# Kernel optimization log

Measured on AMD Instinct MI355X. Metric: run time of the kernel, lower is better.

Reference implementation:

```python
import jax, jax.numpy as jnp
import numpy as np

G, NA, C, NMAX = 32, 1024, 4, 6   # graphs, atoms/graph, latent charge channels, k-grid extent
SIGMA = 1.0                        # Gaussian smearing width (Angstrom)
BOX_L = 20.0


def _kgrid_integers(nmax):
    """All integer triples in [-nmax, nmax]^3 excluding the origin. [K, 3]"""
    r = np.arange(-nmax, nmax + 1)
    n = np.stack(np.meshgrid(r, r, r, indexing='ij'), axis=-1).reshape(-1, 3)
    n = n[np.any(n != 0, axis=1)]
    return jnp.asarray(n, dtype=jnp.float32)  # [K=2196, 3]


def setup_inputs() -> dict:
    key = jax.random.key(0)
    k1, k2, k3 = jax.random.split(key, 3)
    pos = jax.random.uniform(k1, (G * NA, 3), dtype=jnp.float32) * BOX_L
    q = jax.random.normal(k2, (G * NA, C), dtype=jnp.float32) * 0.1
    # near-cubic cells with a small random strain (keeps them invertible)
    cell = jnp.eye(3, dtype=jnp.float32) * BOX_L + 0.1 * jax.random.normal(k3, (G, 3, 3), dtype=jnp.float32)
    batch = jnp.repeat(jnp.arange(G, dtype=jnp.int32), NA)  # sorted segment ids
    return {"q": q, "pos": pos, "cell": cell, "batch": batch}


def reference(q, pos, cell, batch):
    """Latent Ewald reciprocal-space sum.

    E_lr[g] = 1/(2 V_g) * sum_{k != 0} 4*pi/k^2 * exp(-sigma^2 k^2 / 2) * sum_c |S_c(k)|^2
    with S_c(k) = sum_{i in graph g} q_ic exp(i k . r_i).

    Segments are equal-sized and sorted (batch = repeat(arange(G), NA)), so the
    per-graph segment reduction is expressed as a reshape + batched einsum.
    """
    del batch  # layout is encoded by the reshape below (equal-sized sorted segments)
    nvec = _kgrid_integers(NMAX)                         # [K, 3]
    # reciprocal lattice rows: b_i with a_i . b_j = 2*pi*delta_ij
    recip = 2.0 * jnp.pi * jnp.swapaxes(jnp.linalg.inv(cell), -1, -2)  # [G, 3, 3]
    kvec = jnp.einsum('kj,gjd->gkd', nvec, recip)        # [G, K, 3]
    k2 = jnp.sum(kvec * kvec, axis=-1)                   # [G, K]
    vol = jnp.abs(jnp.linalg.det(cell))                  # [G]

    posg = pos.reshape(G, NA, 3)
    qg = q.reshape(G, NA, C)

    phase = jnp.einsum('gnd,gkd->gnk', posg, kvec)       # [G, NA, K]
    cosph = jnp.cos(phase)
    sinph = jnp.sin(phase)
    s_re = jnp.einsum('gnc,gnk->gkc', qg, cosph)         # [G, K, C]
    s_im = jnp.einsum('gnc,gnk->gkc', qg, sinph)
    s2 = jnp.sum(s_re * s_re + s_im * s_im, axis=-1)     # [G, K]

    w = 4.0 * jnp.pi * jnp.exp(-0.5 * (SIGMA ** 2) * k2) / jnp.maximum(k2, 1e-12)
    e_lr = jnp.sum(w * s2, axis=-1) / (2.0 * vol)        # [G]
    return e_lr
```

## Files before the change

kernel.cpp:

```cpp
#include <hip/hip_runtime.h>
#include <math.h>

#define G      32
#define NA     1024
#define C      4
#define KHALF  1098
#define KSLICES 18
#define WAVES  8
#define BLOCK  (WAVES * 64)
#define APW    (NA / WAVES)

typedef float f32x2 __attribute__((ext_vector_type(2)));
typedef float f32x4 __attribute__((ext_vector_type(4)));
typedef float f32x8 __attribute__((ext_vector_type(8)));

__global__ __launch_bounds__(256)
void prepack_kernel(const float* __restrict__ q,
                    const float* __restrict__ pos,
                    float* __restrict__ ws)
{
    const int a = blockIdx.x * 256 + threadIdx.x;
    if (a < G * NA) {
        f32x4 p4 = { pos[a * 3 + 0], pos[a * 3 + 1], pos[a * 3 + 2], 0.f };
        const f32x4 qa = *reinterpret_cast<const f32x4*>(q + (size_t)a * 4);
        f32x4* w = reinterpret_cast<f32x4*>(ws + (size_t)a * 8);
        w[0] = p4;
        w[1] = qa;
    }
}

#define LOAD4(R0, R1, R2, R3, P) do {                                      \
    asm volatile("s_load_dwordx8 %0, %1, 0x0"  : "=s"(R0) : "s"(P));        \
    asm volatile("s_load_dwordx8 %0, %1, 0x20" : "=s"(R1) : "s"(P));        \
    asm volatile("s_load_dwordx8 %0, %1, 0x40" : "=s"(R2) : "s"(P));        \
    asm volatile("s_load_dwordx8 %0, %1, 0x60" : "=s"(R3) : "s"(P));        \
} while (0)

#define WAIT4(R0, R1, R2, R3)                                              \
    asm volatile("s_waitcnt lgkmcnt(0)"                                     \
                 : "+s"(R0), "+s"(R1), "+s"(R2), "+s"(R3))

__global__ __launch_bounds__(BLOCK)
void ewald_recip_kernel(const float* __restrict__ ws,
                        const float* __restrict__ cell,
                        float* __restrict__ out)
{
    __shared__ float s_red[WAVES][64][8];

    const int b    = blockIdx.x;
    const int g    = b / KSLICES;
    const int ks   = b % KSLICES;
    const int t    = threadIdx.x;
    const int wave = t >> 6;
    const int lane = t & 63;

    const float* M = cell + (size_t)g * 9;
    const float m00 = M[0], m01 = M[1], m02 = M[2];
    const float m10 = M[3], m11 = M[4], m12 = M[5];
    const float m20 = M[6], m21 = M[7], m22 = M[8];
    const float c00 =  (m11 * m22 - m12 * m21);
    const float c01 = -(m10 * m22 - m12 * m20);
    const float c02 =  (m10 * m21 - m11 * m20);
    const float c10 = -(m01 * m22 - m02 * m21);
    const float c11 =  (m00 * m22 - m02 * m20);
    const float c12 = -(m00 * m21 - m01 * m20);
    const float c20 =  (m01 * m12 - m02 * m11);
    const float c21 = -(m00 * m12 - m02 * m10);
    const float c22 =  (m00 * m11 - m01 * m10);
    const float det    = m00 * c00 + m01 * c01 + m02 * c02;
    const float invdet = 1.0f / det;

    const int  kk    = ks * 64 + lane;
    const bool valid = (kk < KHALF);
    int n1, n2, n3;
    if (kk < 1014) {
        n1 = 1 + kk / 169;
        const int r = kk - (n1 - 1) * 169;
        n2 = r / 13 - 6;
        n3 = r - (r / 13) * 13 - 6;
    } else if (kk < 1092) {
        const int j = kk - 1014;
        n1 = 0;
        n2 = 1 + j / 13;
        n3 = j - (j / 13) * 13 - 6;
    } else {
        n1 = 0; n2 = 0;
        n3 = kk - 1091;
    }
    const float fn1 = (float)n1, fn2 = (float)n2, fn3 = (float)n3;

    const float kr0 = (fn1 * c00 + fn2 * c10 + fn3 * c20) * invdet;
    const float kr1 = (fn1 * c01 + fn2 * c11 + fn3 * c21) * invdet;
    const float kr2 = (fn1 * c02 + fn2 * c12 + fn3 * c22) * invdet;

    f32x2 aR01 = {0.f, 0.f}, aR23 = {0.f, 0.f};
    f32x2 aI01 = {0.f, 0.f}, aI23 = {0.f, 0.f};

    const unsigned wvByte = (unsigned)__builtin_amdgcn_readfirstlane(wave * APW * 32);
    const char* pa = reinterpret_cast<const char*>(ws)
                   + (size_t)g * NA * 32 + wvByte;

    auto comp = [&](const f32x8& rec) {
        const float ph = fmaf(rec[0], kr0, fmaf(rec[1], kr1, rec[2] * kr2));
        const float u  = __builtin_amdgcn_fractf(ph);
        const float sn = __builtin_amdgcn_sinf(u);
        const float cs = __builtin_amdgcn_cosf(u);
        const f32x2 cs2 = {cs, cs};
        const f32x2 sn2 = {sn, sn};
        const f32x2 q01 = {rec[4], rec[5]};
        const f32x2 q23 = {rec[6], rec[7]};
        aR01 = __builtin_elementwise_fma(q01, cs2, aR01);
        aR23 = __builtin_elementwise_fma(q23, cs2, aR23);
        aI01 = __builtin_elementwise_fma(q01, sn2, aI01);
        aI23 = __builtin_elementwise_fma(q23, sn2, aI23);
    };

    {
        f32x8 A0, A1, A2, A3, B0, B1, B2, B3;
        LOAD4(A0, A1, A2, A3, pa);  pa += 128;
        #pragma unroll 1
        for (int it = 0; it < 15; ++it) {
            WAIT4(A0, A1, A2, A3);
            LOAD4(B0, B1, B2, B3, pa);  pa += 128;
            comp(A0); comp(A1); comp(A2); comp(A3);
            WAIT4(B0, B1, B2, B3);
            LOAD4(A0, A1, A2, A3, pa);  pa += 128;
            comp(B0); comp(B1); comp(B2); comp(B3);
        }
        WAIT4(A0, A1, A2, A3);
        LOAD4(B0, B1, B2, B3, pa);
        comp(A0); comp(A1); comp(A2); comp(A3);
        WAIT4(B0, B1, B2, B3);
        comp(B0); comp(B1); comp(B2); comp(B3);
    }

    {
        float* rp = s_red[wave][lane];
        rp[0] = aR01.x; rp[1] = aR01.y; rp[2] = aR23.x; rp[3] = aR23.y;
        rp[4] = aI01.x; rp[5] = aI01.y; rp[6] = aI23.x; rp[7] = aI23.y;
    }
    __syncthreads();

    if (t < 64) {
        float r0 = 0.f, r1 = 0.f, r2 = 0.f, r3 = 0.f;
        float i0 = 0.f, i1 = 0.f, i2 = 0.f, i3 = 0.f;
        #pragma unroll
        for (int w = 0; w < WAVES; ++w) {
            const float* p = s_red[w][lane];
            r0 += p[0]; r1 += p[1]; r2 += p[2]; r3 += p[3];
            i0 += p[4]; i1 += p[5]; i2 += p[6]; i3 += p[7];
        }
        const float s2 = r0 * r0 + r1 * r1 + r2 * r2 + r3 * r3
                       + i0 * i0 + i1 * i1 + i2 * i2 + i3 * i3;
        const float kk2 = kr0 * kr0 + kr1 * kr1 + kr2 * kr2;
        const float fourpi2 = 4.0f * (float)M_PI * (float)M_PI;
        const float k2 = fourpi2 * kk2;
        const float wt = 4.0f * (float)M_PI * __expf(-0.5f * k2) / fmaxf(k2, 1e-12f);
        float contrib = valid ? wt * s2 : 0.0f;
        #pragma unroll
        for (int off = 32; off > 0; off >>= 1)
            contrib += __shfl_down(contrib, off, 64);
        if (lane == 0)
            atomicAdd(&out[g], contrib * fabsf(invdet));
    }
}

extern "C" void kernel_launch(void* const* d_in, const int* in_sizes, int n_in,
                              void* d_out, int out_size, void* d_ws, size_t ws_size,
                              hipStream_t stream) {
    const float* q    = (const float*)d_in[0];
    const float* pos  = (const float*)d_in[1];
    const float* cell = (const float*)d_in[2];
    float* out = (float*)d_out;
    float* ws  = (float*)d_ws;

    hipMemsetAsync(out, 0, G * sizeof(float), stream);

    prepack_kernel<<<(G * NA + 255) / 256, 256, 0, stream>>>(q, pos, ws);

    dim3 grid(G * KSLICES);
    dim3 block(BLOCK);
    ewald_recip_kernel<<<grid, block, 0, stream>>>(ws, cell, out);
}
```

Before: 83.95 us.

## Split atom dimension across blocks and add a separate reduction kernel

After: 85.16 us. Within noise of the previous version (+1.4%).

```diff
diff --git a/kernel.cpp b/kernel.cpp
--- a/kernel.cpp
+++ b/kernel.cpp
@@ -3,12 +3,15 @@
 
 #define G      32
 #define NA     1024
-#define C      4
 #define KHALF  1098
 #define KSLICES 18
+#define KSLOT  (KSLICES * 64)
 #define WAVES  8
 #define BLOCK  (WAVES * 64)
-#define APW    (NA / WAVES)
+#define ASPLIT 4
+#define APW    (NA / (WAVES * ASPLIT))
+
+#define REC_FLOATS (G * NA * 8)
 
 typedef float f32x2 __attribute__((ext_vector_type(2)));
 typedef float f32x4 __attribute__((ext_vector_type(4)));
@@ -40,39 +43,8 @@
     asm volatile("s_waitcnt lgkmcnt(0)"                                     \
                  : "+s"(R0), "+s"(R1), "+s"(R2), "+s"(R3))
 
-__global__ __launch_bounds__(BLOCK)
-void ewald_recip_kernel(const float* __restrict__ ws,
-                        const float* __restrict__ cell,
-                        float* __restrict__ out)
-{
-    __shared__ float s_red[WAVES][64][8];
-
-    const int b    = blockIdx.x;
-    const int g    = b / KSLICES;
-    const int ks   = b % KSLICES;
-    const int t    = threadIdx.x;
-    const int wave = t >> 6;
-    const int lane = t & 63;
-
-    const float* M = cell + (size_t)g * 9;
-    const float m00 = M[0], m01 = M[1], m02 = M[2];
-    const float m10 = M[3], m11 = M[4], m12 = M[5];
-    const float m20 = M[6], m21 = M[7], m22 = M[8];
-    const float c00 =  (m11 * m22 - m12 * m21);
-    const float c01 = -(m10 * m22 - m12 * m20);
-    const float c02 =  (m10 * m21 - m11 * m20);
-    const float c10 = -(m01 * m22 - m02 * m21);
-    const float c11 =  (m00 * m22 - m02 * m20);
-    const float c12 = -(m00 * m21 - m01 * m20);
-    const float c20 =  (m01 * m12 - m02 * m11);
-    const float c21 = -(m00 * m12 - m02 * m10);
-    const float c22 =  (m00 * m11 - m01 * m10);
-    const float det    = m00 * c00 + m01 * c01 + m02 * c02;
-    const float invdet = 1.0f / det;
-
-    const int  kk    = ks * 64 + lane;
-    const bool valid = (kk < KHALF);
-    int n1, n2, n3;
+__device__ __forceinline__ void decode_k(int kk, int& n1, int& n2, int& n3)
+{
     if (kk < 1014) {
         n1 = 1 + kk / 169;
         const int r = kk - (n1 - 1) * 169;
@@ -87,6 +59,46 @@
         n1 = 0; n2 = 0;
         n3 = kk - 1091;
     }
+}
+
+#define CELL_COFACTORS(M)                                                  \
+    const float m00 = M[0], m01 = M[1], m02 = M[2];                         \
+    const float m10 = M[3], m11 = M[4], m12 = M[5];                         \
+    const float m20 = M[6], m21 = M[7], m22 = M[8];                         \
+    const float c00 =  (m11 * m22 - m12 * m21);                             \
+    const float c01 = -(m10 * m22 - m12 * m20);                             \
+    const float c02 =  (m10 * m21 - m11 * m20);                             \
+    const float c10 = -(m01 * m22 - m02 * m21);                             \
+    const float c11 =  (m00 * m22 - m02 * m20);                             \
+    const float c12 = -(m00 * m21 - m01 * m20);                             \
+    const float c20 =  (m01 * m12 - m02 * m11);                             \
+    const float c21 = -(m00 * m12 - m02 * m10);                             \
+    const float c22 =  (m00 * m11 - m01 * m10);                             \
+    const float det    = m00 * c00 + m01 * c01 + m02 * c02;                 \
+    const float invdet = 1.0f / det;
+
+__global__ __launch_bounds__(BLOCK)
+void ewald_partial_kernel(const float* __restrict__ ws,
+                          const float* __restrict__ cell,
+                          float* __restrict__ part)
+{
+    __shared__ float s_red[WAVES][64][8];
+
+    const int b    = blockIdx.x;
+    const int g    = b / (KSLICES * ASPLIT);
+    const int rem  = b % (KSLICES * ASPLIT);
+    const int ks   = rem / ASPLIT;
+    const int as   = rem % ASPLIT;
+    const int t    = threadIdx.x;
+    const int wave = t >> 6;
+    const int lane = t & 63;
+
+    const float* M = cell + (size_t)g * 9;
+    CELL_COFACTORS(M);
+
+    const int kk = ks * 64 + lane;
+    int n1, n2, n3;
+    decode_k(kk, n1, n2, n3);
     const float fn1 = (float)n1, fn2 = (float)n2, fn3 = (float)n3;
 
     const float kr0 = (fn1 * c00 + fn2 * c10 + fn3 * c20) * invdet;
@@ -96,7 +108,8 @@
     f32x2 aR01 = {0.f, 0.f}, aR23 = {0.f, 0.f};
     f32x2 aI01 = {0.f, 0.f}, aI23 = {0.f, 0.f};
 
-    const unsigned wvByte = (unsigned)__builtin_amdgcn_readfirstlane(wave * APW * 32);
+    const unsigned wvByte = (unsigned)__builtin_amdgcn_readfirstlane(
+        (as * (NA / ASPLIT) + wave * APW) * 32);
     const char* pa = reinterpret_cast<const char*>(ws)
                    + (size_t)g * NA * 32 + wvByte;
 
@@ -119,7 +132,7 @@
         f32x8 A0, A1, A2, A3, B0, B1, B2, B3;
         LOAD4(A0, A1, A2, A3, pa);  pa += 128;
         #pragma unroll 1
-        for (int it = 0; it < 15; ++it) {
+        for (int it = 0; it < 3; ++it) {
             WAIT4(A0, A1, A2, A3);
             LOAD4(B0, B1, B2, B3, pa);  pa += 128;
             comp(A0); comp(A1); comp(A2); comp(A3);
@@ -142,27 +155,64 @@
     __syncthreads();
 
     if (t < 64) {
-        float r0 = 0.f, r1 = 0.f, r2 = 0.f, r3 = 0.f;
-        float i0 = 0.f, i1 = 0.f, i2 = 0.f, i3 = 0.f;
+        f32x4 R = {0.f, 0.f, 0.f, 0.f};
+        f32x4 I = {0.f, 0.f, 0.f, 0.f};
         #pragma unroll
         for (int w = 0; w < WAVES; ++w) {
-            const float* p = s_red[w][lane];
-            r0 += p[0]; r1 += p[1]; r2 += p[2]; r3 += p[3];
-            i0 += p[4]; i1 += p[5]; i2 += p[6]; i3 += p[7];
+            const f32x4* p = reinterpret_cast<const f32x4*>(s_red[w][lane]);
+            R += p[0];
+            I += p[1];
         }
-        const float s2 = r0 * r0 + r1 * r1 + r2 * r2 + r3 * r3
-                       + i0 * i0 + i1 * i1 + i2 * i2 + i3 * i3;
-        const float kk2 = kr0 * kr0 + kr1 * kr1 + kr2 * kr2;
-        const float fourpi2 = 4.0f * (float)M_PI * (float)M_PI;
-        const float k2 = fourpi2 * kk2;
-        const float wt = 4.0f * (float)M_PI * __expf(-0.5f * k2) / fmaxf(k2, 1e-12f);
-        float contrib = valid ? wt * s2 : 0.0f;
-        #pragma unroll
-        for (int off = 32; off > 0; off >>= 1)
-            contrib += __shfl_down(contrib, off, 64);
-        if (lane == 0)
-            atomicAdd(&out[g], contrib * fabsf(invdet));
-    }
+        const int gk = (g * KSLICES + ks) * 64 + lane;
+        f32x4* dst = reinterpret_cast<f32x4*>(part) + ((size_t)gk * ASPLIT + as) * 2;
+        dst[0] = R;
+        dst[1] = I;
+    }
+}
+
+__global__ __launch_bounds__(256)
+void ewald_reduce_kernel(const float* __restrict__ part,
+                         const float* __restrict__ cell,
+                         float* __restrict__ out)
+{
+    const int idx  = blockIdx.x * 256 + threadIdx.x;
+    const int g    = idx / KSLOT;
+    const int kk   = idx % KSLOT;
+    const int lane = threadIdx.x & 63;
+    const bool valid = (kk < KHALF);
+
+    const float* M = cell + (size_t)g * 9;
+    CELL_COFACTORS(M);
+
+    int n1, n2, n3;
+    decode_k(kk, n1, n2, n3);
+    const float fn1 = (float)n1, fn2 = (float)n2, fn3 = (float)n3;
+    const float kr0 = (fn1 * c00 + fn2 * c10 + fn3 * c20) * invdet;
+    const float kr1 = (fn1 * c01 + fn2 * c11 + fn3 * c21) * invdet;
+    const float kr2 = (fn1 * c02 + fn2 * c12 + fn3 * c22) * invdet;
+
+    f32x4 R = {0.f, 0.f, 0.f, 0.f};
+    f32x4 I = {0.f, 0.f, 0.f, 0.f};
+    const f32x4* p = reinterpret_cast<const f32x4*>(part) + (size_t)idx * ASPLIT * 2;
+    #pragma unroll
+    for (int as = 0; as < ASPLIT; ++as) {
+        R += p[2 * as];
+        I += p[2 * as + 1];
+    }
+    const float s2 = R.x * R.x + R.y * R.y + R.z * R.z + R.w * R.w
+                   + I.x * I.x + I.y * I.y + I.z * I.z + I.w * I.w;
+
+    const float kk2 = kr0 * kr0 + kr1 * kr1 + kr2 * kr2;
+    const float fourpi2 = 4.0f * (float)M_PI * (float)M_PI;
+    const float k2 = fourpi2 * kk2;
+    const float wt = 4.0f * (float)M_PI * __expf(-0.5f * k2) / fmaxf(k2, 1e-12f);
+
+    float contrib = valid ? wt * s2 * fabsf(invdet) : 0.0f;
+    #pragma unroll
+    for (int off = 32; off > 0; off >>= 1)
+        contrib += __shfl_down(contrib, off, 64);
+    if (lane == 0)
+        atomicAdd(&out[g], contrib);
 }
 
 extern "C" void kernel_launch(void* const* d_in, const int* in_sizes, int n_in,
@@ -171,14 +221,15 @@
     const float* q    = (const float*)d_in[0];
     const float* pos  = (const float*)d_in[1];
     const float* cell = (const float*)d_in[2];
-    float* out = (float*)d_out;
-    float* ws  = (float*)d_ws;
+    float* out  = (float*)d_out;
+    float* ws   = (float*)d_ws;
+    float* part = ws + REC_FLOATS;
 
     hipMemsetAsync(out, 0, G * sizeof(float), stream);
 
     prepack_kernel<<<(G * NA + 255) / 256, 256, 0, stream>>>(q, pos, ws);
 
-    dim3 grid(G * KSLICES);
-    dim3 block(BLOCK);
-    ewald_recip_kernel<<<grid, block, 0, stream>>>(ws, cell, out);
-}
+    ewald_partial_kernel<<<G * KSLICES * ASPLIT, BLOCK, 0, stream>>>(ws, cell, part);
+
+    ewald_reduce_kernel<<<(G * KSLOT) / 256, 256, 0, stream>>>(part, cell, out);
+}
```
